# Kernel tuning notes

Measured on AMD Instinct MI355X. Metric: run time of the kernel, lower is better.

## Reference

```python
import jax, jax.numpy as jnp
import numpy as np

B, T, C = 2, 2048, 1024
NUM_HEADS = 16
HEAD_DIM = C // NUM_HEADS
TEMP = 1.0
LN_EPS = 1e-6


def setup_inputs() -> dict:
    key = jax.random.key(0)
    kx, kqw, kpw = jax.random.split(key, 3)
    x = jax.random.normal(kx, (B, T, C), dtype=jnp.float32)
    # causal mask, broadcastable to [B, H, T, T]
    mask = jnp.tril(jnp.ones((T, T), dtype=bool))[None, None, :, :]
    # LayerNorm params (flax defaults: scale=1, bias=0)
    ln_scale = jnp.ones((C,), dtype=jnp.float32)
    ln_bias = jnp.zeros((C,), dtype=jnp.float32)
    # xavier_uniform init for dense kernels, zero bias (torch_linear)
    lim_qkv = float(np.sqrt(6.0 / (C + 3 * C)))
    qkv_w = jax.random.uniform(kqw, (C, 3 * C), jnp.float32, -lim_qkv, lim_qkv)
    qkv_b = jnp.zeros((3 * C,), dtype=jnp.float32)
    lim_p = float(np.sqrt(6.0 / (C + C)))
    proj_w = jax.random.uniform(kpw, (C, C), jnp.float32, -lim_p, lim_p)
    proj_b = jnp.zeros((C,), dtype=jnp.float32)
    return {"x": x, "mask": mask, "ln_scale": ln_scale, "ln_bias": ln_bias,
            "qkv_w": qkv_w, "qkv_b": qkv_b, "proj_w": proj_w, "proj_b": proj_b}


def reference(x, mask, ln_scale, ln_bias, qkv_w, qkv_b, proj_w, proj_b):
    b, t, c = x.shape
    # LayerNorm (eps=1e-6, flax default)
    mu = jnp.mean(x, axis=-1, keepdims=True)
    var = jnp.mean(jnp.square(x - mu), axis=-1, keepdims=True)
    xn = (x - mu) * jax.lax.rsqrt(var + LN_EPS) * ln_scale + ln_bias
    # fused QKV projection
    qkv = xn @ qkv_w + qkv_b
    q, k, v = jnp.split(qkv, 3, axis=-1)
    q = q.reshape(b, t, NUM_HEADS, HEAD_DIM) / TEMP
    k = k.reshape(b, t, NUM_HEADS, HEAD_DIM)
    v = v.reshape(b, t, NUM_HEADS, HEAD_DIM)
    # scaled dot-product attention with mask (eval path: no dropout)
    q = q / jnp.sqrt(jnp.float32(HEAD_DIM)).astype(x.dtype)
    scores = jnp.einsum('bqhd,bkhd->bhqk', q, k)  # [B,H,T,T]
    big_neg = jnp.finfo(x.dtype).min
    scores = jnp.where(mask, scores, big_neg)
    attn_weights = jax.nn.softmax(scores, axis=-1).astype(x.dtype)
    out = jnp.einsum('bhqk,bkhd->bqhd', attn_weights, v).reshape(b, t, c)
    return out @ proj_w + proj_b
```

## Files before the change

### kernel.cpp

```cpp
#include <hip/hip_runtime.h>
#include <cstdint>
#include <math.h>

#define DEV __device__ __forceinline__

typedef unsigned int u32;
typedef unsigned short u16;
typedef __attribute__((ext_vector_type(4))) float f32x4;
typedef __attribute__((ext_vector_type(4))) u32 u32x4;
typedef __attribute__((ext_vector_type(2))) u32 u32x2;
typedef __attribute__((ext_vector_type(8))) __bf16 bf16x8;

static_assert(sizeof(bf16x8) == 16, "bf16x8 must be 16B");

static constexpr int Tn = 2048, Cn = 1024;
static constexpr int Mrows = 2 * Tn;
static constexpr float QSCALE2 = 0.125f * 1.44269504088896f;

DEV u16 f2bf_rne(float f) {
  u32 u = __builtin_bit_cast(u32, f);
  u32 r = u + 0x7fffu + ((u >> 16) & 1u);
  return (u16)(r >> 16);
}
DEV float bf2f(u16 h) {
  u32 u = ((u32)h) << 16;
  return __builtin_bit_cast(float, u);
}
DEV u32 pack2bf(float a, float b) {
  return (u32)f2bf_rne(a) | ((u32)f2bf_rne(b) << 16);
}
DEV float fexp2(float x) {
#if __has_builtin(__builtin_amdgcn_exp2f)
  return __builtin_amdgcn_exp2f(x);
#else
  return exp2f(x);
#endif
}

DEV void stage16(const void* g, void* l) {
#if __has_builtin(__builtin_amdgcn_global_load_lds)
  __builtin_amdgcn_global_load_lds(
      (__attribute__((address_space(1))) u32*)(uintptr_t)g,
      (__attribute__((address_space(3))) u32*)l, 16, 0, 0);
#else
  *(u32x4*)l = *(const u32x4*)g;
#endif
}

__global__ __launch_bounds__(256) void ln_kernel(const float* __restrict__ x,
                                                 const float* __restrict__ sc,
                                                 const float* __restrict__ bi,
                                                 u16* __restrict__ xn) {
  int row = blockIdx.x;
  int t = threadIdx.x;
  const float* xr = x + (size_t)row * Cn;
  f32x4 v = *(const f32x4*)(xr + t * 4);
  float s = v.x + v.y + v.z + v.w;
  float s2 = v.x * v.x + v.y * v.y + v.z * v.z + v.w * v.w;
#pragma unroll
  for (int off = 1; off < 64; off <<= 1) {
    s += __shfl_xor(s, off);
    s2 += __shfl_xor(s2, off);
  }
  __shared__ float red[8];
  if ((t & 63) == 0) {
    red[(t >> 6) * 2] = s;
    red[(t >> 6) * 2 + 1] = s2;
  }
  __syncthreads();
  s = red[0] + red[2] + red[4] + red[6];
  s2 = red[1] + red[3] + red[5] + red[7];
  float mean = s * (1.0f / Cn);
  float var = s2 * (1.0f / Cn) - mean * mean;
  float rstd = rsqrtf(var + 1e-6f);
  f32x4 g = *(const f32x4*)(sc + t * 4);
  f32x4 b = *(const f32x4*)(bi + t * 4);
  u32 lo = pack2bf((v.x - mean) * rstd * g.x + b.x, (v.y - mean) * rstd * g.y + b.y);
  u32 hi = pack2bf((v.z - mean) * rstd * g.z + b.z, (v.w - mean) * rstd * g.w + b.w);
  u32x2 pack = {lo, hi};
  *(u32x2*)(xn + (size_t)row * Cn + t * 4) = pack;
}

__global__ __launch_bounds__(256) void transpose_cast2(const float* __restrict__ qkv_w,
                                                       u16* __restrict__ wqkv,
                                                       const float* __restrict__ proj_w,
                                                       u16* __restrict__ wproj) {
  __shared__ float tile[32][33];
  int bx = blockIdx.x;
  const float* src;
  u16* dst;
  int Cc;
  if (bx < 96) {
    src = qkv_w; dst = wqkv; Cc = 3072;
  } else {
    src = proj_w; dst = wproj; Cc = 1024; bx -= 96;
  }
  int tx = threadIdx.x, ty = threadIdx.y;
  int c0 = bx * 32, r0 = blockIdx.y * 32;
#pragma unroll
  for (int k = 0; k < 4; ++k)
    tile[ty + 8 * k][tx] = src[(size_t)(r0 + ty + 8 * k) * Cc + c0 + tx];
  __syncthreads();
#pragma unroll
  for (int k = 0; k < 4; ++k)
    dst[(size_t)(c0 + ty + 8 * k) * 1024 + r0 + tx] = f2bf_rne(tile[tx][ty + 8 * k]);
}

__global__ __launch_bounds__(256) void vt_prep(const u16* __restrict__ qkvm,
                                               u16* __restrict__ vt) {
  __shared__ u16 tile[32][33];
  int bh = blockIdx.z;
  int b = bh >> 4, h = bh & 15;
  int t0 = blockIdx.x * 32, d0 = blockIdx.y * 32;
  int tx = threadIdx.x, ty = threadIdx.y;
#pragma unroll
  for (int k = 0; k < 4; ++k)
    tile[ty + 8 * k][tx] =
        qkvm[(size_t)(b * Tn + t0 + ty + 8 * k) * 3072 + 2 * Cn + h * 64 + d0 + tx];
  __syncthreads();
#pragma unroll
  for (int k = 0; k < 4; ++k)
    vt[((size_t)bh * 64 + d0 + ty + 8 * k) * 2048 + t0 + tx] = tile[tx][ty + 8 * k];
}

template <bool OUT_F32, bool QKV_SCALE>
__global__ __launch_bounds__(256, 3) void gemm_kernel(const u16* __restrict__ A,
                                                      const u16* __restrict__ Bt,
                                                      const float* __restrict__ bias,
                                                      void* __restrict__ Cout,
                                                      int Nsz, int Ksz) {
  __shared__ u16 As[128 * 32];
  __shared__ u16 Bs[128 * 32];
  int t = threadIdx.x;
  int l = t & 63, w = t >> 6;
  int quad = l >> 4, c16 = l & 15;
  int wm = w & 1, wn = w >> 1;
  int m0 = blockIdx.y * 128, n0 = blockIdx.x * 128;

  f32x4 acc[4][4];
#pragma unroll
  for (int mt = 0; mt < 4; ++mt)
#pragma unroll
    for (int nt = 0; nt < 4; ++nt) acc[mt][nt] = (f32x4){0.f, 0.f, 0.f, 0.f};

  for (int kk = 0; kk < Ksz; kk += 32) {
#pragma unroll
    for (int i = 0; i < 2; ++i) {
      int c = t + i * 256;
      int m = c >> 2, k8 = (c & 3) ^ ((m >> 1) & 3);
      stage16(A + (size_t)(m0 + m) * Ksz + kk + k8 * 8, (char*)As + c * 16);
    }
#pragma unroll
    for (int i = 0; i < 2; ++i) {
      int c = t + i * 256;
      int n = c >> 2, k8 = (c & 3) ^ ((n >> 1) & 3);
      stage16(Bt + (size_t)(n0 + n) * Ksz + kk + k8 * 8, (char*)Bs + c * 16);
    }
    __syncthreads();
    bf16x8 af[4], bf[4];
#pragma unroll
    for (int mt = 0; mt < 4; ++mt) {
      int m = wm * 64 + mt * 16 + c16;
      int LC = m * 4 + (quad ^ ((m >> 1) & 3));
      af[mt] = *(const bf16x8*)((const char*)As + LC * 16);
    }
#pragma unroll
    for (int nt = 0; nt < 4; ++nt) {
      int n = wn * 64 + nt * 16 + c16;
      int LC = n * 4 + (quad ^ ((n >> 1) & 3));
      bf[nt] = *(const bf16x8*)((const char*)Bs + LC * 16);
    }
#pragma unroll
    for (int mt = 0; mt < 4; ++mt)
#pragma unroll
      for (int nt = 0; nt < 4; ++nt)
        acc[mt][nt] = __builtin_amdgcn_mfma_f32_16x16x32_bf16(af[mt], bf[nt],
                                                              acc[mt][nt], 0, 0, 0);
    __syncthreads();
  }
#pragma unroll
  for (int mt = 0; mt < 4; ++mt) {
    int row = m0 + wm * 64 + mt * 16 + quad * 4;
#pragma unroll
    for (int nt = 0; nt < 4; ++nt) {
      int col = n0 + wn * 64 + nt * 16 + c16;
      float bv = bias[col];
      float scale = (QKV_SCALE && col < 1024) ? QSCALE2 : 1.0f;
#pragma unroll
      for (int r = 0; r < 4; ++r) {
        float v = (acc[mt][nt][r] + bv) * scale;
        if (OUT_F32)
          ((float*)Cout)[(size_t)(row + r) * Nsz + col] = v;
        else
          ((u16*)Cout)[(size_t)(row + r) * Nsz + col] = f2bf_rne(v);
      }
    }
  }
}

__constant__ int4 chunk_tab[24] = {
    {15, 0, 8, 0}, {15, 8, 8, 1}, {14, 0, 8, 0}, {7, 0, 8, -1},
    {14, 8, 7, 1}, {13, 0, 7, 0}, {13, 7, 7, 1}, {12, 0, 7, 0}, {6, 0, 7, -1},
    {12, 7, 6, 1}, {11, 0, 6, 0}, {11, 6, 6, 1}, {10, 0, 6, 0}, {5, 0, 6, -1},
    {10, 6, 5, 1}, {9, 0, 5, 0}, {9, 5, 5, 1}, {8, 0, 5, 0}, {4, 0, 5, -1},
    {8, 5, 4, 1}, {3, 0, 4, -1},
    {2, 0, 3, -1},
    {1, 0, 2, -1},
    {0, 0, 1, -1}};

__global__ __launch_bounds__(256, 2) void flash_kernel(const u16* __restrict__ qkv,
                                                       const u16* __restrict__ vt,
                                                       u16* __restrict__ aout,
                                                       u16* __restrict__ Op,
                                                       float* __restrict__ ml) {
  int4 ck = chunk_tab[blockIdx.x >> 5];
  int bh = blockIdx.x & 31;
  int qt = ck.x, k0 = ck.y, kend = ck.y + ck.z, half = ck.w;
  int b = bh >> 4, h = bh & 15;
  int t = threadIdx.x, l = t & 63, w = t >> 6;
  int quad = l >> 4, c16 = l & 15;
  int q0 = qt * 128;

  __shared__ u16 Ks[128 * 64];
  __shared__ u16 Vs[64 * 128];
  __shared__ u16 Ps[128 * 64];

  bf16x8 qf[2][2];
#pragma unroll
  for (int nt = 0; nt < 2; ++nt)
#pragma unroll
    for (int ks = 0; ks < 2; ++ks)
      qf[nt][ks] = *(const bf16x8*)(qkv +
          (size_t)(b * Tn + q0 + w * 32 + nt * 16 + c16) * 3072 +
          h * 64 + ks * 32 + quad * 8);

  float mrow[2] = {-1e30f, -1e30f};
  float lrow[2] = {0.f, 0.f};
  f32x4 o[2][4];
#pragma unroll
  for (int mq = 0; mq < 2; ++mq)
#pragma unroll
    for (int dt = 0; dt < 4; ++dt) o[mq][dt] = (f32x4){0.f, 0.f, 0.f, 0.f};

  for (int kt = k0; kt < kend; ++kt) {
#pragma unroll
    for (int i = 0; i < 4; ++i) {
      int c = t + i * 256;
      int key = c >> 3, d8 = (c & 7) ^ (key & 7);
      stage16(qkv + (size_t)(b * Tn + kt * 128 + key) * 3072 + Cn + h * 64 + d8 * 8,
              (char*)Ks + c * 16);
    }
#pragma unroll
    for (int i = 0; i < 4; ++i) {
      int c = t + i * 256;
      int d = c >> 4, k8 = (c & 15) ^ (d & 15);
      stage16(vt + ((size_t)bh * 64 + d) * 2048 + kt * 128 + k8 * 8,
              (char*)Vs + c * 16);
    }
    __syncthreads();

    f32x4 s[8][2];
#pragma unroll
    for (int mt = 0; mt < 8; ++mt)
#pragma unroll
      for (int nt = 0; nt < 2; ++nt) s[mt][nt] = (f32x4){0.f, 0.f, 0.f, 0.f};
#pragma unroll
    for (int mt = 0; mt < 8; ++mt) {
#pragma unroll
      for (int ks = 0; ks < 2; ++ks) {
        int key = mt * 16 + c16;
        int d8 = ks * 4 + quad;
        int LC = key * 8 + (d8 ^ (key & 7));
        bf16x8 kf = *(const bf16x8*)((const char*)Ks + LC * 16);
#pragma unroll
        for (int nt = 0; nt < 2; ++nt)
          s[mt][nt] = __builtin_amdgcn_mfma_f32_16x16x32_bf16(kf, qf[nt][ks],
                                                              s[mt][nt], 0, 0, 0);
      }
    }
    if (kt == qt) {
#pragma unroll
      for (int mt = 0; mt < 8; ++mt)
#pragma unroll
        for (int nt = 0; nt < 2; ++nt)
#pragma unroll
          for (int r = 0; r < 4; ++r) {
            int key = kt * 128 + mt * 16 + quad * 4 + r;
            int q = q0 + w * 32 + nt * 16 + c16;
            if (key > q) s[mt][nt][r] = -1e30f;
          }
    }
    float alph[2];
#pragma unroll
    for (int nt = 0; nt < 2; ++nt) {
      float rm = -1e30f;
#pragma unroll
      for (int mt = 0; mt < 8; ++mt)
#pragma unroll
        for (int r = 0; r < 4; ++r) rm = fmaxf(rm, s[mt][nt][r]);
      rm = fmaxf(rm, __shfl_xor(rm, 16));
      rm = fmaxf(rm, __shfl_xor(rm, 32));
      float mnew = fmaxf(mrow[nt], rm);
      alph[nt] = fexp2(mrow[nt] - mnew);
      mrow[nt] = mnew;
      float rs = 0.f;
#pragma unroll
      for (int mt = 0; mt < 8; ++mt)
#pragma unroll
        for (int r = 0; r < 4; ++r) {
          float e = fexp2(s[mt][nt][r] - mnew);
          s[mt][nt][r] = e;
          rs += e;
        }
      rs += __shfl_xor(rs, 16);
      rs += __shfl_xor(rs, 32);
      lrow[nt] = lrow[nt] * alph[nt] + rs;
    }
#pragma unroll
    for (int mq = 0; mq < 2; ++mq)
#pragma unroll
      for (int r = 0; r < 4; ++r) {
        float a = __shfl(alph[mq], quad * 4 + r);
#pragma unroll
        for (int dt = 0; dt < 4; ++dt) o[mq][dt][r] *= a;
      }
#pragma unroll
    for (int ksh = 0; ksh < 2; ++ksh) {
#pragma unroll
      for (int mtl = 0; mtl < 4; ++mtl) {
        int mt = ksh * 4 + mtl;
#pragma unroll
        for (int nt = 0; nt < 2; ++nt) {
          int q = w * 32 + nt * 16 + c16;
          int c8 = mtl * 2 + (quad >> 1);
          u32x2 pk = {pack2bf(s[mt][nt][0], s[mt][nt][1]),
                      pack2bf(s[mt][nt][2], s[mt][nt][3])};
          *(u32x2*)((char*)Ps + q * 128 + ((c8 ^ (c16 & 7)) * 16) + (quad & 1) * 8) =
              pk;
        }
      }
#pragma unroll
      for (int ksl = 0; ksl < 2; ++ksl) {
        int ks = ksh * 2 + ksl;
        bf16x8 pa[2];
#pragma unroll
        for (int mq = 0; mq < 2; ++mq) {
          int q = w * 32 + mq * 16 + c16;
          int c8 = ksl * 4 + quad;
          pa[mq] = *(const bf16x8*)((const char*)Ps + q * 128 +
                                    ((c8 ^ (c16 & 7)) * 16));
        }
#pragma unroll
        for (int dt = 0; dt < 4; ++dt) {
          int d = dt * 16 + c16;
          int vc = d * 16 + ((ks * 4 + quad) ^ (d & 15));
          bf16x8 vf = *(const bf16x8*)((const char*)Vs + vc * 16);
#pragma unroll
          for (int mq = 0; mq < 2; ++mq)
            o[mq][dt] = __builtin_amdgcn_mfma_f32_16x16x32_bf16(pa[mq], vf,
                                                                o[mq][dt], 0, 0, 0);
        }
      }
    }
    __syncthreads();
  }

  float linv[2] = {1.0f / lrow[0], 1.0f / lrow[1]};
  if (half < 0) {
#pragma unroll
    for (int mq = 0; mq < 2; ++mq)
#pragma unroll
      for (int r = 0; r < 4; ++r) {
        float li = __shfl(linv[mq], quad * 4 + r);
        int q = q0 + w * 32 + mq * 16 + quad * 4 + r;
#pragma unroll
        for (int dt = 0; dt < 4; ++dt)
          aout[(size_t)(b * Tn + q) * 1024 + h * 64 + dt * 16 + c16] =
              f2bf_rne(o[mq][dt][r] * li);
      }
  } else {
    int ps = ((qt - 8) * 32 + bh) * 2 + half;
#pragma unroll
    for (int mq = 0; mq < 2; ++mq)
#pragma unroll
      for (int r = 0; r < 4; ++r) {
        float li = __shfl(linv[mq], quad * 4 + r);
        int qr = w * 32 + mq * 16 + quad * 4 + r;
#pragma unroll
        for (int dt = 0; dt < 4; ++dt)
          Op[((size_t)ps * 128 + qr) * 64 + dt * 16 + c16] =
              f2bf_rne(o[mq][dt][r] * li);
      }
    if (quad == 0) {
#pragma unroll
      for (int nt = 0; nt < 2; ++nt) {
        int qr = w * 32 + nt * 16 + c16;
        ml[((size_t)ps * 128 + qr) * 2] = mrow[nt];
        ml[((size_t)ps * 128 + qr) * 2 + 1] = lrow[nt];
      }
    }
  }
}

__global__ __launch_bounds__(256) void combine_kernel(const u16* __restrict__ Op,
                                                      const float* __restrict__ ml,
                                                      u16* __restrict__ aout) {
  int qt = 8 + (blockIdx.x >> 5);
  int bh = blockIdx.x & 31;
  int b = bh >> 4, h = bh & 15;
  int ps0 = ((qt - 8) * 32 + bh) * 2;
  int d = threadIdx.x & 63, rq = threadIdx.x >> 6;
  for (int r = 0; r < 32; ++r) {
    int row = rq * 32 + r;
    float m0 = ml[((size_t)ps0 * 128 + row) * 2];
    float l0 = ml[((size_t)ps0 * 128 + row) * 2 + 1];
    float m1 = ml[((size_t)(ps0 + 1) * 128 + row) * 2];
    float l1 = ml[((size_t)(ps0 + 1) * 128 + row) * 2 + 1];
    float M = fmaxf(m0, m1);
    float w0 = fexp2(m0 - M) * l0, w1 = fexp2(m1 - M) * l1;
    float inv = 1.0f / (w0 + w1);
    float o0 = bf2f(Op[((size_t)ps0 * 128 + row) * 64 + d]);
    float o1 = bf2f(Op[((size_t)(ps0 + 1) * 128 + row) * 64 + d]);
    aout[(size_t)(b * Tn + qt * 128 + row) * 1024 + h * 64 + d] =
        f2bf_rne((w0 * o0 + w1 * o1) * inv);
  }
}

extern "C" void kernel_launch(void* const* d_in, const int* in_sizes, int n_in,
                              void* d_out, int out_size, void* d_ws, size_t ws_size,
                              hipStream_t stream) {
  const float* x = (const float*)d_in[0];
  const float* ln_s = (const float*)d_in[2];
  const float* ln_b = (const float*)d_in[3];
  const float* qkv_w = (const float*)d_in[4];
  const float* qkv_b = (const float*)d_in[5];
  const float* proj_w = (const float*)d_in[6];
  const float* proj_b = (const float*)d_in[7];
  float* out = (float*)d_out;
  char* ws = (char*)d_ws;

  u16* xn = (u16*)ws;
  u16* wqkv = (u16*)(ws + (8ull << 20));
  u16* wproj = (u16*)(ws + (14ull << 20));
  u16* qkvm = (u16*)(ws + (16ull << 20));
  u16* attn = (u16*)(ws + (40ull << 20));
  u16* vt = (u16*)(ws + (48ull << 20));
  u16* Op = (u16*)ws;
  float* ml = (float*)(ws + (8ull << 20));

  ln_kernel<<<Mrows, 256, 0, stream>>>(x, ln_s, ln_b, xn);
  transpose_cast2<<<dim3(128, 32), dim3(32, 8), 0, stream>>>(qkv_w, wqkv, proj_w,
                                                             wproj);
  gemm_kernel<false, true><<<dim3(24, 32), 256, 0, stream>>>(xn, wqkv, qkv_b, qkvm,
                                                             3072, 1024);
  vt_prep<<<dim3(64, 2, 32), dim3(32, 8), 0, stream>>>(qkvm, vt);
  flash_kernel<<<768, 256, 0, stream>>>(qkvm, vt, attn, Op, ml);
  combine_kernel<<<256, 256, 0, stream>>>(Op, ml, attn);
  gemm_kernel<true, false><<<dim3(8, 32), 256, 0, stream>>>(attn, wproj, proj_b, out,
                                                            1024, 1024);
}
```

Baseline: 220.8 us.

## Double-buffer K tiles, read V from global, finer causal split with lazy rescale

The flash kernel now double-buffers K tiles in LDS, prefetching the next tile while the current one is computed. V fragments are read straight from global (L2) instead of being staged in LDS, which shrinks the P buffer. Work is split into smaller chunks (up to 3 partials per query tile, over 31 chunk types) for better load balance, and the combine kernel is extended to merge 2 or 3 partials. The online softmax also skips rescaling unless the row max grows by more than a threshold, and uses a hardware bf16 pack instruction; together these reduce ALU and LDS traffic at the cost of extra global V reads and more partial writes.

Result: slower. 249.8 us (+13.1%).

```diff
diff --git a/kernel.cpp b/kernel.cpp
--- a/kernel.cpp
+++ b/kernel.cpp
@@ -28,6 +28,11 @@
 }
 DEV u32 pack2bf(float a, float b) {
   return (u32)f2bf_rne(a) | ((u32)f2bf_rne(b) << 16);
+}
+DEV u32 cvtpk(float lo, float hi) {
+  u32 r;
+  asm("v_cvt_pk_bf16_f32 %0, %1, %2" : "=v"(r) : "v"(lo), "v"(hi));
+  return r;
 }
 DEV float fexp2(float x) {
 #if __has_builtin(__builtin_amdgcn_exp2f)
@@ -198,15 +203,21 @@
   }
 }
 
-__constant__ int4 chunk_tab[24] = {
-    {15, 0, 8, 0}, {15, 8, 8, 1}, {14, 0, 8, 0}, {7, 0, 8, -1},
-    {14, 8, 7, 1}, {13, 0, 7, 0}, {13, 7, 7, 1}, {12, 0, 7, 0}, {6, 0, 7, -1},
-    {12, 7, 6, 1}, {11, 0, 6, 0}, {11, 6, 6, 1}, {10, 0, 6, 0}, {5, 0, 6, -1},
-    {10, 6, 5, 1}, {9, 0, 5, 0}, {9, 5, 5, 1}, {8, 0, 5, 0}, {4, 0, 5, -1},
-    {8, 5, 4, 1}, {3, 0, 4, -1},
-    {2, 0, 3, -1},
+__constant__ int4 chunk_tab[31] = {
+    {15, 0, 6, 0},  {10, 0, 6, 15}, {5, 0, 6, -1},
+    {15, 6, 5, 1},  {15, 11, 5, 2}, {14, 0, 5, 3},  {14, 5, 5, 4},
+    {14, 10, 5, 5}, {13, 0, 5, 6},  {13, 5, 5, 7},  {12, 0, 5, 9},
+    {10, 6, 5, 16}, {9, 0, 5, 17},  {9, 5, 5, 18},  {8, 0, 5, 19},
+    {4, 0, 5, -1},
+    {13, 10, 4, 8}, {12, 5, 4, 10}, {12, 9, 4, 11}, {11, 0, 4, 12},
+    {11, 4, 4, 13}, {11, 8, 4, 14}, {8, 5, 4, 20},  {7, 0, 4, 21},
+    {7, 4, 4, 22},  {6, 0, 4, 23},  {3, 0, 4, -1},
+    {6, 4, 3, 24},  {2, 0, 3, -1},
     {1, 0, 2, -1},
     {0, 0, 1, -1}};
+
+__constant__ int2 comb_tab[10] = {{23, 2}, {21, 2}, {19, 2}, {17, 2}, {15, 2},
+                                  {12, 3}, {9, 3},  {6, 3},  {3, 3},  {0, 3}};
 
 __global__ __launch_bounds__(256, 2) void flash_kernel(const u16* __restrict__ qkv,
                                                        const u16* __restrict__ vt,
@@ -215,15 +226,14 @@
                                                        float* __restrict__ ml) {
   int4 ck = chunk_tab[blockIdx.x >> 5];
   int bh = blockIdx.x & 31;
-  int qt = ck.x, k0 = ck.y, kend = ck.y + ck.z, half = ck.w;
+  int qt = ck.x, k0 = ck.y, nk = ck.z, slot = ck.w;
   int b = bh >> 4, h = bh & 15;
   int t = threadIdx.x, l = t & 63, w = t >> 6;
   int quad = l >> 4, c16 = l & 15;
   int q0 = qt * 128;
 
-  __shared__ u16 Ks[128 * 64];
-  __shared__ u16 Vs[64 * 128];
-  __shared__ u16 Ps[128 * 64];
+  __shared__ u16 Ks[2][128 * 64];
+  __shared__ u16 Ps[128 * 32];
 
   bf16x8 qf[2][2];
 #pragma unroll
@@ -234,6 +244,11 @@
           (size_t)(b * Tn + q0 + w * 32 + nt * 16 + c16) * 3072 +
           h * 64 + ks * 32 + quad * 8);
 
+  const u16* vb[4];
+#pragma unroll
+  for (int dt = 0; dt < 4; ++dt)
+    vb[dt] = vt + ((size_t)bh * 64 + dt * 16 + c16) * 2048 + quad * 8;
+
   float mrow[2] = {-1e30f, -1e30f};
   float lrow[2] = {0.f, 0.f};
   f32x4 o[2][4];
@@ -242,22 +257,28 @@
 #pragma unroll
     for (int dt = 0; dt < 4; ++dt) o[mq][dt] = (f32x4){0.f, 0.f, 0.f, 0.f};
 
-  for (int kt = k0; kt < kend; ++kt) {
-#pragma unroll
-    for (int i = 0; i < 4; ++i) {
-      int c = t + i * 256;
-      int key = c >> 3, d8 = (c & 7) ^ (key & 7);
-      stage16(qkv + (size_t)(b * Tn + kt * 128 + key) * 3072 + Cn + h * 64 + d8 * 8,
-              (char*)Ks + c * 16);
-    }
-#pragma unroll
-    for (int i = 0; i < 4; ++i) {
-      int c = t + i * 256;
-      int d = c >> 4, k8 = (c & 15) ^ (d & 15);
-      stage16(vt + ((size_t)bh * 64 + d) * 2048 + kt * 128 + k8 * 8,
-              (char*)Vs + c * 16);
-    }
-    __syncthreads();
+#pragma unroll
+  for (int i = 0; i < 4; ++i) {
+    int c = t + i * 256;
+    int key = c >> 3, d8 = (c & 7) ^ (key & 7);
+    stage16(qkv + (size_t)(b * Tn + k0 * 128 + key) * 3072 + Cn + h * 64 + d8 * 8,
+            (char*)Ks[0] + c * 16);
+  }
+  __syncthreads();
+
+  for (int it = 0; it < nk; ++it) {
+    int kt = k0 + it;
+    if (it + 1 < nk) {
+#pragma unroll
+      for (int i = 0; i < 4; ++i) {
+        int c = t + i * 256;
+        int key = c >> 3, d8 = (c & 7) ^ (key & 7);
+        stage16(qkv + (size_t)(b * Tn + (kt + 1) * 128 + key) * 3072 + Cn +
+                    h * 64 + d8 * 8,
+                (char*)Ks[(it + 1) & 1] + c * 16);
+      }
+    }
+    const char* Kb = (const char*)Ks[it & 1];
 
     f32x4 s[8][2];
 #pragma unroll
@@ -271,7 +292,7 @@
         int key = mt * 16 + c16;
         int d8 = ks * 4 + quad;
         int LC = key * 8 + (d8 ^ (key & 7));
-        bf16x8 kf = *(const bf16x8*)((const char*)Ks + LC * 16);
+        bf16x8 kf = *(const bf16x8*)(Kb + LC * 16);
 #pragma unroll
         for (int nt = 0; nt < 2; ++nt)
           s[mt][nt] = __builtin_amdgcn_mfma_f32_16x16x32_bf16(kf, qf[nt][ks],
@@ -291,82 +312,87 @@
           }
     }
     float alph[2];
+    int needv[2];
 #pragma unroll
     for (int nt = 0; nt < 2; ++nt) {
-      float rm = -1e30f;
+      float m8[8];
 #pragma unroll
       for (int mt = 0; mt < 8; ++mt)
-#pragma unroll
-        for (int r = 0; r < 4; ++r) rm = fmaxf(rm, s[mt][nt][r]);
+        m8[mt] = fmaxf(fmaxf(s[mt][nt][0], s[mt][nt][1]),
+                       fmaxf(s[mt][nt][2], s[mt][nt][3]));
+      float rm = fmaxf(fmaxf(fmaxf(m8[0], m8[1]), fmaxf(m8[2], m8[3])),
+                       fmaxf(fmaxf(m8[4], m8[5]), fmaxf(m8[6], m8[7])));
       rm = fmaxf(rm, __shfl_xor(rm, 16));
       rm = fmaxf(rm, __shfl_xor(rm, 32));
-      float mnew = fmaxf(mrow[nt], rm);
-      alph[nt] = fexp2(mrow[nt] - mnew);
+      int need = __any(rm > mrow[nt] + 6.0f);
+      needv[nt] = need;
+      float mnew = need ? fmaxf(mrow[nt], rm) : mrow[nt];
+      alph[nt] = need ? fexp2(mrow[nt] - mnew) : 1.0f;
       mrow[nt] = mnew;
-      float rs = 0.f;
-#pragma unroll
-      for (int mt = 0; mt < 8; ++mt)
-#pragma unroll
-        for (int r = 0; r < 4; ++r) {
-          float e = fexp2(s[mt][nt][r] - mnew);
-          s[mt][nt][r] = e;
-          rs += e;
-        }
+      float part[8];
+#pragma unroll
+      for (int mt = 0; mt < 8; ++mt) {
+        float e0 = fexp2(s[mt][nt][0] - mnew);
+        float e1 = fexp2(s[mt][nt][1] - mnew);
+        float e2 = fexp2(s[mt][nt][2] - mnew);
+        float e3 = fexp2(s[mt][nt][3] - mnew);
+        s[mt][nt][0] = e0; s[mt][nt][1] = e1;
+        s[mt][nt][2] = e2; s[mt][nt][3] = e3;
+        part[mt] = (e0 + e1) + (e2 + e3);
+      }
+      float rs = ((part[0] + part[1]) + (part[2] + part[3])) +
+                 ((part[4] + part[5]) + (part[6] + part[7]));
       rs += __shfl_xor(rs, 16);
       rs += __shfl_xor(rs, 32);
       lrow[nt] = lrow[nt] * alph[nt] + rs;
     }
 #pragma unroll
     for (int mq = 0; mq < 2; ++mq)
-#pragma unroll
-      for (int r = 0; r < 4; ++r) {
-        float a = __shfl(alph[mq], quad * 4 + r);
-#pragma unroll
-        for (int dt = 0; dt < 4; ++dt) o[mq][dt][r] *= a;
-      }
-#pragma unroll
-    for (int ksh = 0; ksh < 2; ++ksh) {
-#pragma unroll
-      for (int mtl = 0; mtl < 4; ++mtl) {
-        int mt = ksh * 4 + mtl;
+      if (needv[mq]) {
+#pragma unroll
+        for (int r = 0; r < 4; ++r) {
+          float a = __shfl(alph[mq], quad * 4 + r);
+#pragma unroll
+          for (int dt = 0; dt < 4; ++dt) o[mq][dt][r] *= a;
+        }
+      }
+#pragma unroll
+    for (int ksq = 0; ksq < 4; ++ksq) {
+      bf16x8 vf[4];
+#pragma unroll
+      for (int dt = 0; dt < 4; ++dt)
+        vf[dt] = *(const bf16x8*)(vb[dt] + kt * 128 + ksq * 32);
+#pragma unroll
+      for (int mtp = 0; mtp < 2; ++mtp) {
+        int mt = ksq * 2 + mtp;
 #pragma unroll
         for (int nt = 0; nt < 2; ++nt) {
           int q = w * 32 + nt * 16 + c16;
-          int c8 = mtl * 2 + (quad >> 1);
-          u32x2 pk = {pack2bf(s[mt][nt][0], s[mt][nt][1]),
-                      pack2bf(s[mt][nt][2], s[mt][nt][3])};
-          *(u32x2*)((char*)Ps + q * 128 + ((c8 ^ (c16 & 7)) * 16) + (quad & 1) * 8) =
-              pk;
+          int g = (mtp * 2 + (quad >> 1)) ^ (c16 & 3);
+          u32x2 pk = {cvtpk(s[mt][nt][0], s[mt][nt][1]),
+                      cvtpk(s[mt][nt][2], s[mt][nt][3])};
+          *(u32x2*)((char*)Ps + q * 64 + g * 16 + (quad & 1) * 8) = pk;
         }
       }
-#pragma unroll
-      for (int ksl = 0; ksl < 2; ++ksl) {
-        int ks = ksh * 2 + ksl;
-        bf16x8 pa[2];
-#pragma unroll
-        for (int mq = 0; mq < 2; ++mq) {
-          int q = w * 32 + mq * 16 + c16;
-          int c8 = ksl * 4 + quad;
-          pa[mq] = *(const bf16x8*)((const char*)Ps + q * 128 +
-                                    ((c8 ^ (c16 & 7)) * 16));
-        }
-#pragma unroll
-        for (int dt = 0; dt < 4; ++dt) {
-          int d = dt * 16 + c16;
-          int vc = d * 16 + ((ks * 4 + quad) ^ (d & 15));
-          bf16x8 vf = *(const bf16x8*)((const char*)Vs + vc * 16);
-#pragma unroll
-          for (int mq = 0; mq < 2; ++mq)
-            o[mq][dt] = __builtin_amdgcn_mfma_f32_16x16x32_bf16(pa[mq], vf,
-                                                                o[mq][dt], 0, 0, 0);
-        }
-      }
+      bf16x8 pa[2];
+#pragma unroll
+      for (int mq = 0; mq < 2; ++mq) {
+        int q = w * 32 + mq * 16 + c16;
+        pa[mq] = *(const bf16x8*)((const char*)Ps + q * 64 +
+                                  ((quad ^ (c16 & 3)) * 16));
+      }
+#pragma unroll
+      for (int dt = 0; dt < 4; ++dt)
+#pragma unroll
+        for (int mq = 0; mq < 2; ++mq)
+          o[mq][dt] = __builtin_amdgcn_mfma_f32_16x16x32_bf16(pa[mq], vf[dt],
+                                                              o[mq][dt], 0, 0, 0);
     }
     __syncthreads();
   }
 
   float linv[2] = {1.0f / lrow[0], 1.0f / lrow[1]};
-  if (half < 0) {
+  if (slot < 0) {
 #pragma unroll
     for (int mq = 0; mq < 2; ++mq)
 #pragma unroll
@@ -379,7 +405,7 @@
               f2bf_rne(o[mq][dt][r] * li);
       }
   } else {
-    int ps = ((qt - 8) * 32 + bh) * 2 + half;
+    int ps = slot * 32 + bh;
 #pragma unroll
     for (int mq = 0; mq < 2; ++mq)
 #pragma unroll
@@ -405,24 +431,30 @@
 __global__ __launch_bounds__(256) void combine_kernel(const u16* __restrict__ Op,
                                                       const float* __restrict__ ml,
                                                       u16* __restrict__ aout) {
-  int qt = 8 + (blockIdx.x >> 5);
+  int qt = 6 + (blockIdx.x >> 5);
   int bh = blockIdx.x & 31;
   int b = bh >> 4, h = bh & 15;
-  int ps0 = ((qt - 8) * 32 + bh) * 2;
+  int2 cb = comb_tab[qt - 6];
+  int base = cb.x, n = cb.y;
   int d = threadIdx.x & 63, rq = threadIdx.x >> 6;
   for (int r = 0; r < 32; ++r) {
     int row = rq * 32 + r;
-    float m0 = ml[((size_t)ps0 * 128 + row) * 2];
-    float l0 = ml[((size_t)ps0 * 128 + row) * 2 + 1];
-    float m1 = ml[((size_t)(ps0 + 1) * 128 + row) * 2];
-    float l1 = ml[((size_t)(ps0 + 1) * 128 + row) * 2 + 1];
-    float M = fmaxf(m0, m1);
-    float w0 = fexp2(m0 - M) * l0, w1 = fexp2(m1 - M) * l1;
-    float inv = 1.0f / (w0 + w1);
-    float o0 = bf2f(Op[((size_t)ps0 * 128 + row) * 64 + d]);
-    float o1 = bf2f(Op[((size_t)(ps0 + 1) * 128 + row) * 64 + d]);
+    float mv[3], lv[3], ov[3];
+#pragma unroll
+    for (int i = 0; i < 3; ++i) {
+      int ps = (base + (i < n ? i : 0)) * 32 + bh;
+      bool valid = i < n;
+      mv[i] = valid ? ml[((size_t)ps * 128 + row) * 2] : -1e30f;
+      lv[i] = valid ? ml[((size_t)ps * 128 + row) * 2 + 1] : 0.f;
+      ov[i] = valid ? bf2f(Op[((size_t)ps * 128 + row) * 64 + d]) : 0.f;
+    }
+    float M = fmaxf(fmaxf(mv[0], mv[1]), mv[2]);
+    float w0 = fexp2(mv[0] - M) * lv[0];
+    float w1 = fexp2(mv[1] - M) * lv[1];
+    float w2 = fexp2(mv[2] - M) * lv[2];
+    float inv = 1.0f / (w0 + w1 + w2);
     aout[(size_t)(b * Tn + qt * 128 + row) * 1024 + h * 64 + d] =
-        f2bf_rne((w0 * o0 + w1 * o1) * inv);
+        f2bf_rne((w0 * ov[0] + w1 * ov[1] + w2 * ov[2]) * inv);
   }
 }
 
@@ -446,7 +478,7 @@
   u16* attn = (u16*)(ws + (40ull << 20));
   u16* vt = (u16*)(ws + (48ull << 20));
   u16* Op = (u16*)ws;
-  float* ml = (float*)(ws + (8ull << 20));
+  float* ml = (float*)(ws + (13ull << 20));
 
   ln_kernel<<<Mrows, 256, 0, stream>>>(x, ln_s, ln_b, xn);
   transpose_cast2<<<dim3(128, 32), dim3(32, 8), 0, stream>>>(qkv_w, wqkv, proj_w,
@@ -454,8 +486,8 @@
   gemm_kernel<false, true><<<dim3(24, 32), 256, 0, stream>>>(xn, wqkv, qkv_b, qkvm,
                                                              3072, 1024);
   vt_prep<<<dim3(64, 2, 32), dim3(32, 8), 0, stream>>>(qkvm, vt);
-  flash_kernel<<<768, 256, 0, stream>>>(qkvm, vt, attn, Op, ml);
-  combine_kernel<<<256, 256, 0, stream>>>(Op, ml, attn);
+  flash_kernel<<<992, 256, 0, stream>>>(qkvm, vt, attn, Op, ml);
+  combine_kernel<<<320, 256, 0, stream>>>(Op, ml, attn);
   gemm_kernel<true, false><<<dim3(8, 32), 256, 0, stream>>>(attn, wproj, proj_b, out,
                                                             1024, 1024);
 }
```
